# Optimization experiments

Hardware: AMD Instinct MI355X
Metric: run time of the kernel (lower is better)

The kernel has to match this reference:

```python
import jax, jax.numpy as jnp
import numpy as np

HEADS = 8
DIM_HEAD = 64
SCALE = DIM_HEAD ** -0.5
QUERY_DIM = 512
CTX_DIM = 64
INNER = HEADS * DIM_HEAD  # 512
GATE_HID = 32


def setup_inputs() -> dict:
    key = jax.random.key(0)
    ks = jax.random.split(key, 11)
    B, N, M = 4, 2048, 2048
    s = lambda fan: 1.0 / np.sqrt(fan)
    return {
        "x": jax.random.normal(ks[0], (B, N, QUERY_DIM), dtype=jnp.float32),
        "context": jax.random.normal(ks[1], (B, M, CTX_DIM), dtype=jnp.float32),
        "Wq": jax.random.normal(ks[2], (QUERY_DIM, INNER), dtype=jnp.float32) * s(QUERY_DIM),
        "Wk": jax.random.normal(ks[3], (CTX_DIM, INNER), dtype=jnp.float32) * s(CTX_DIM),
        "Wv": jax.random.normal(ks[4], (CTX_DIM, INNER), dtype=jnp.float32) * s(CTX_DIM),
        "W1": jax.random.normal(ks[5], (CTX_DIM, GATE_HID), dtype=jnp.float32) * s(CTX_DIM),
        "b1": jnp.zeros((GATE_HID,), dtype=jnp.float32),
        "W2": jax.random.normal(ks[6], (GATE_HID, 1), dtype=jnp.float32) * s(GATE_HID),
        "b2": jnp.zeros((1,), dtype=jnp.float32),
        "Wo": jax.random.normal(ks[7], (INNER, QUERY_DIM), dtype=jnp.float32) * s(INNER),
        "bo": jnp.zeros((QUERY_DIM,), dtype=jnp.float32),
    }


def reference(x, context, Wq, Wk, Wv, W1, b1, W2, b2, Wo, bo):
    B, N, _ = x.shape
    M = context.shape[1]
    # visual reliability gate: sigmoid(relu(ctx @ W1 + b1) @ W2 + b2) -> [B, M, 1]
    gate = jax.nn.sigmoid(jax.nn.relu(context @ W1 + b1) @ W2 + b2)
    ctx = context * gate
    # projections
    q = (x @ Wq).reshape(B, N, HEADS, DIM_HEAD).transpose(0, 2, 1, 3)    # [B,H,N,D]
    k = (ctx @ Wk).reshape(B, M, HEADS, DIM_HEAD).transpose(0, 2, 1, 3)  # [B,H,M,D]
    v = (ctx @ Wv).reshape(B, M, HEADS, DIM_HEAD).transpose(0, 2, 1, 3)  # [B,H,M,D]
    # scaled dot-product attention (full score matrix, as in source)
    sim = jnp.einsum('bhid,bhjd->bhij', q, k) * SCALE
    attn = jax.nn.softmax(sim, axis=-1)
    out = jnp.einsum('bhij,bhjd->bhid', attn, v)
    out = out.transpose(0, 2, 1, 3).reshape(B, N, INNER)
    return out @ Wo + bo
```

## Files before the change

kernel.cpp:

```cpp
#include <hip/hip_runtime.h>

typedef unsigned short u16;
typedef unsigned int u32;
using frag16 = __attribute__((ext_vector_type(8))) short;
using facc   = __attribute__((ext_vector_type(4))) float;
using facc16 = __attribute__((ext_vector_type(16))) float;

#define DEV static __device__ __forceinline__

DEV u16 f2bf(float f) {
  union { float f; unsigned u; } v; v.f = f;
  unsigned r = v.u + 0x7fffu + ((v.u >> 16) & 1u);
  return (u16)(r >> 16);
}
DEV unsigned fbits(float f) {
  union { float f; unsigned u; } v; v.f = f;
  return v.u;
}
DEV unsigned pkbf(float lo, float hi) {
  return __builtin_amdgcn_perm(fbits(hi) + 0x8000u, fbits(lo) + 0x8000u, 0x07060302u);
}
DEV void gld16(const u16* g, u16* l) {
  __builtin_amdgcn_global_load_lds(
      (__attribute__((address_space(1))) unsigned int*)(g),
      (__attribute__((address_space(3))) unsigned int*)(l), 16, 0, 0);
}

__global__ __launch_bounds__(256) void wtrans_all(
    const float* __restrict__ Wq, const float* __restrict__ Wk,
    const float* __restrict__ Wv, const float* __restrict__ Wo,
    u16* __restrict__ WqT, u16* __restrict__ WkT,
    u16* __restrict__ WvT, u16* __restrict__ WoT) {
  int id = blockIdx.x * 256 + threadIdx.x;
  const float* W; u16* WT; int K, idx;
  if (id < 262144)      { W = Wq; WT = WqT; K = 512; idx = id; }
  else if (id < 294912) { W = Wk; WT = WkT; K = 64;  idx = id - 262144; }
  else if (id < 327680) { W = Wv; WT = WvT; K = 64;  idx = id - 294912; }
  else                  { W = Wo; WT = WoT; K = 512; idx = id - 327680; }
  int n = idx / K, k = idx - n * K;
  WT[idx] = f2bf(W[k * 512 + n]);
}

__global__ void cvt_kernel(const float4* __restrict__ x, u16* __restrict__ xb, int n4) {
  int id = blockIdx.x * 256 + threadIdx.x;
  if (id >= n4) return;
  float4 v = x[id];
  ushort4 o;
  o.x = f2bf(v.x); o.y = f2bf(v.y); o.z = f2bf(v.z); o.w = f2bf(v.w);
  *(ushort4*)(xb + (size_t)id * 4) = o;
}

__global__ __launch_bounds__(256) void gate_kernel(const float* __restrict__ ctx,
    const float* __restrict__ W1, const float* __restrict__ b1,
    const float* __restrict__ W2, const float* __restrict__ b2,
    u16* __restrict__ gctx) {
  int wave = threadIdx.x >> 6, lane = threadIdx.x & 63;
  int row = blockIdx.x * 4 + wave;
  __shared__ float sc[4][64];
  float cv = ctx[(size_t)row * 64 + lane];
  sc[wave][lane] = cv;
  __syncthreads();
  float h = 0.f;
  if (lane < 32) {
    h = b1[lane];
    #pragma unroll
    for (int i = 0; i < 64; ++i) h += sc[wave][i] * W1[i * 32 + lane];
    h = fmaxf(h, 0.f) * W2[lane];
  }
  #pragma unroll
  for (int off = 32; off; off >>= 1) h += __shfl_xor(h, off);
  float g = 1.f / (1.f + __expf(-(h + b2[0])));
  gctx[(size_t)row * 64 + lane] = f2bf(cv * g);
}

template<int MODE>
__global__ __launch_bounds__(256) void gemm128(const u16* __restrict__ A,
    const u16* __restrict__ BT, void* __restrict__ Cp,
    const float* __restrict__ bias, int N, float scale) {
  const int K = 512;
  const int lane = threadIdx.x & 63, wave = threadIdx.x >> 6;
  const int quad = lane >> 4, l16 = lane & 15;
  const int wr = wave >> 1, wc = wave & 1;
  const int m0 = blockIdx.y * 128, n0 = blockIdx.x * 64;

  __shared__ __align__(16) u16 As[128 * 32];
  __shared__ __align__(16) u16 Bs[64 * 32];

  const u16* gA = A + (size_t)(m0 + wave * 32 + (lane >> 2)) * K + (lane & 3) * 8;
  const u16* gB = BT + (size_t)(n0 + wave * 16 + (lane >> 2)) * K + (lane & 3) * 8;
  u16* lA0 = As + wave * 1024;
  u16* lA1 = As + wave * 1024 + 512;
  u16* lB  = Bs + wave * 512;

  facc acc[4][2] = {};

  for (int k0 = 0; k0 < K; k0 += 32) {
    if (k0) __syncthreads();
    gld16(gA + k0, lA0);
    gld16(gA + 16 * K + k0, lA1);
    gld16(gB + k0, lB);
    __syncthreads();

    frag16 af[4], bf[2];
    #pragma unroll
    for (int rt = 0; rt < 4; ++rt)
      af[rt] = *(const frag16*)(As + (wr * 64 + rt * 16 + l16) * 32 + quad * 8);
    #pragma unroll
    for (int ct = 0; ct < 2; ++ct)
      bf[ct] = *(const frag16*)(Bs + (wc * 32 + ct * 16 + l16) * 32 + quad * 8);
    #pragma unroll
    for (int rt = 0; rt < 4; ++rt)
      #pragma unroll
      for (int ct = 0; ct < 2; ++ct)
        acc[rt][ct] = __builtin_amdgcn_mfma_f32_16x16x32_bf16(af[rt], bf[ct], acc[rt][ct], 0, 0, 0);
  }

  #pragma unroll
  for (int rt = 0; rt < 4; ++rt) {
    #pragma unroll
    for (int ct = 0; ct < 2; ++ct) {
      int col = n0 + wc * 32 + ct * 16 + l16;
      int r0g = m0 + wr * 64 + rt * 16 + quad * 4;
      if (MODE == 0) {
        u16* C = (u16*)Cp;
        #pragma unroll
        for (int r = 0; r < 4; ++r)
          C[(size_t)(r0g + r) * N + col] = f2bf(acc[rt][ct][r] * scale);
      } else {
        float* C = (float*)Cp;
        float bv = bias[col];
        #pragma unroll
        for (int r = 0; r < 4; ++r)
          C[(size_t)(r0g + r) * N + col] = acc[rt][ct][r] + bv;
      }
    }
  }
}

template<int MODE>
__global__ __launch_bounds__(256) void gemm_bt(const u16* __restrict__ A,
    const u16* __restrict__ BT, void* __restrict__ Cp, int M, int N, int K) {
  int lane = threadIdx.x & 63, wave = threadIdx.x >> 6;
  int quad = lane >> 4, l16 = lane & 15;
  int wr = wave >> 1, wc = wave & 1;
  int rowBase = blockIdx.y * 64 + wr * 32;
  int colBase = blockIdx.x * 64 + wc * 32;
  facc acc[2][2] = {};
  const u16* a0 = A + (size_t)(rowBase + l16) * K + quad * 8;
  const u16* a1 = a0 + (size_t)16 * K;
  const u16* b0 = BT + (size_t)(colBase + l16) * K + quad * 8;
  const u16* b1p = b0 + (size_t)16 * K;
  for (int kk = 0; kk < K; kk += 32) {
    frag16 af0 = *(const frag16*)(a0 + kk);
    frag16 af1 = *(const frag16*)(a1 + kk);
    frag16 bf0 = *(const frag16*)(b0 + kk);
    frag16 bf1 = *(const frag16*)(b1p + kk);
    acc[0][0] = __builtin_amdgcn_mfma_f32_16x16x32_bf16(af0, bf0, acc[0][0], 0, 0, 0);
    acc[0][1] = __builtin_amdgcn_mfma_f32_16x16x32_bf16(af0, bf1, acc[0][1], 0, 0, 0);
    acc[1][0] = __builtin_amdgcn_mfma_f32_16x16x32_bf16(af1, bf0, acc[1][0], 0, 0, 0);
    acc[1][1] = __builtin_amdgcn_mfma_f32_16x16x32_bf16(af1, bf1, acc[1][1], 0, 0, 0);
  }
  #pragma unroll
  for (int rt = 0; rt < 2; ++rt) {
    #pragma unroll
    for (int ct = 0; ct < 2; ++ct) {
      int col = colBase + ct * 16 + l16;
      int r0g = rowBase + rt * 16 + quad * 4;
      if (MODE == 3) {
        u16* C = (u16*)Cp;
        int hh = col >> 6, d = col & 63;
        int b = r0g >> 11;
        #pragma unroll
        for (int r = 0; r < 4; ++r) {
          int m = (r0g + r) & 2047;
          size_t addr = ((((size_t)(b * 8 + hh) * 64 + (m >> 5)) * 4 + (d >> 4)) * 64
                         + ((d >> 3) & 1) * 32 + (m & 31)) * 8 + (d & 7);
          C[addr] = f2bf(acc[rt][ct][r]);
        }
      } else {
        u16* C = (u16*)Cp;
        int hh = col >> 6, d = col & 63;
        int b = r0g >> 11;
        int m = r0g & 2047;
        size_t addr = ((((size_t)(b * 8 + hh) * 64 + (m >> 5)) * 4
                        + ((m >> 4) & 1) * 2 + (d >> 5)) * 64
                       + ((m >> 3) & 1) * 32 + (d & 31)) * 8 + (m & 7);
        ushort4 o;
        o.x = f2bf(acc[rt][ct][0]); o.y = f2bf(acc[rt][ct][1]);
        o.z = f2bf(acc[rt][ct][2]); o.w = f2bf(acc[rt][ct][3]);
        *(ushort4*)(C + addr) = o;
      }
    }
  }
}

__global__ __launch_bounds__(256, 3) void attn_kernel(
    const u16* __restrict__ qb, const u16* __restrict__ Kp,
    const u16* __restrict__ Vp, float* __restrict__ Opart,
    float* __restrict__ Lpart) {
  const int lane = threadIdx.x & 63, wave = threadIdx.x >> 6;
  const int l32 = lane & 31;
  const int hi = lane >> 5;
  const int bid = blockIdx.x;
  const int bh = bid & 31;
  const int qblk = (bid >> 5) & 15;
  const int js = bid >> 9;
  const int b = bh >> 3, h = bh & 7;
  const int q0 = (qblk * 4 + wave) * 32;
  const int rowg = b * 2048 + q0 + l32;

  const u16* qp = qb + (size_t)rowg * 512 + h * 64 + hi * 8;
  frag16 qf0 = *(const frag16*)(qp);
  frag16 qf1 = *(const frag16*)(qp + 16);
  frag16 qf2 = *(const frag16*)(qp + 32);
  frag16 qf3 = *(const frag16*)(qp + 48);

  facc16 O0 = {}, O1 = {};
  float lsum = 0.f;

  const size_t ts = 2048;
  const u16* kpb = Kp + (size_t)(bh * 64 + js * 32) * ts + lane * 8;
  const u16* vpb = Vp + (size_t)(bh * 64 + js * 32) * ts + lane * 8;

  for (int t = 0; t < 32; ++t) {
    const u16* kt = kpb + (size_t)t * ts;
    frag16 kf0 = *(const frag16*)(kt);
    frag16 kf1 = *(const frag16*)(kt + 512);
    frag16 kf2 = *(const frag16*)(kt + 1024);
    frag16 kf3 = *(const frag16*)(kt + 1536);
    const u16* vt = vpb + (size_t)t * ts;
    frag16 vf00 = *(const frag16*)(vt);
    frag16 vf01 = *(const frag16*)(vt + 512);
    frag16 vf10 = *(const frag16*)(vt + 1024);
    frag16 vf11 = *(const frag16*)(vt + 1536);

    facc16 S = {};
    S = __builtin_amdgcn_mfma_f32_32x32x16_bf16(kf0, qf0, S, 0, 0, 0);
    S = __builtin_amdgcn_mfma_f32_32x32x16_bf16(kf1, qf1, S, 0, 0, 0);
    S = __builtin_amdgcn_mfma_f32_32x32x16_bf16(kf2, qf2, S, 0, 0, 0);
    S = __builtin_amdgcn_mfma_f32_32x32x16_bf16(kf3, qf3, S, 0, 0, 0);

    float e[16];
    #pragma unroll
    for (int r = 0; r < 16; ++r) e[r] = __builtin_amdgcn_exp2f(S[r]);
    #pragma unroll
    for (int r = 0; r < 16; ++r) lsum += e[r];

    unsigned pu[2][4];
    #pragma unroll
    for (int c = 0; c < 2; ++c) {
      const float* ee = e + c * 8;
      unsigned L0 = pkbf(ee[0], ee[1]);
      unsigned L1 = pkbf(ee[2], ee[3]);
      unsigned H0 = pkbf(ee[4], ee[5]);
      unsigned H1 = pkbf(ee[6], ee[7]);
      unsigned Y0 = hi ? L0 : H0;
      unsigned Y1 = hi ? L1 : H1;
      unsigned X0 = (unsigned)__shfl_xor((int)Y0, 32);
      unsigned X1 = (unsigned)__shfl_xor((int)Y1, 32);
      pu[c][0] = hi ? X0 : L0;
      pu[c][1] = hi ? X1 : L1;
      pu[c][2] = hi ? H0 : X0;
      pu[c][3] = hi ? H1 : X1;
    }
    frag16 P0 = *(frag16*)&pu[0][0];
    frag16 P1 = *(frag16*)&pu[1][0];

    O0 = __builtin_amdgcn_mfma_f32_32x32x16_bf16(vf00, P0, O0, 0, 0, 0);
    O0 = __builtin_amdgcn_mfma_f32_32x32x16_bf16(vf10, P1, O0, 0, 0, 0);
    O1 = __builtin_amdgcn_mfma_f32_32x32x16_bf16(vf01, P0, O1, 0, 0, 0);
    O1 = __builtin_amdgcn_mfma_f32_32x32x16_bf16(vf11, P1, O1, 0, 0, 0);
  }

  lsum += __shfl_xor(lsum, 32);

  float* op = Opart + ((size_t)js * 8192 + rowg) * 512 + h * 64;
  #pragma unroll
  for (int dt = 0; dt < 2; ++dt) {
    #pragma unroll
    for (int rq = 0; rq < 4; ++rq) {
      float4 v;
      if (dt == 0) { v.x = O0[rq*4]; v.y = O0[rq*4+1]; v.z = O0[rq*4+2]; v.w = O0[rq*4+3]; }
      else         { v.x = O1[rq*4]; v.y = O1[rq*4+1]; v.z = O1[rq*4+2]; v.w = O1[rq*4+3]; }
      int d0 = dt * 32 + 8 * rq + 4 * hi;
      *(float4*)(op + d0) = v;
    }
  }
  if (!hi) Lpart[(size_t)js * 65536 + (size_t)rowg * 8 + h] = lsum;
}

__global__ __launch_bounds__(256) void combine_kernel(const float* __restrict__ Opart,
    const float* __restrict__ Lpart, u16* __restrict__ ob) {
  int id = blockIdx.x * 256 + threadIdx.x;
  int row = id >> 7, c4 = (id & 127) * 4;
  int hh = c4 >> 6;
  size_t o = (size_t)row * 512 + c4;
  const float4 o0 = *(const float4*)(Opart + o);
  const float4 o1 = *(const float4*)(Opart + (size_t)8192 * 512 + o);
  float rl = 1.f / (Lpart[(size_t)row * 8 + hh] + Lpart[65536 + (size_t)row * 8 + hh]);
  ushort4 u;
  u.x = f2bf((o0.x + o1.x) * rl);
  u.y = f2bf((o0.y + o1.y) * rl);
  u.z = f2bf((o0.z + o1.z) * rl);
  u.w = f2bf((o0.w + o1.w) * rl);
  *(ushort4*)(ob + o) = u;
}

extern "C" void kernel_launch(void* const* d_in, const int* in_sizes, int n_in,
                              void* d_out, int out_size, void* d_ws, size_t ws_size,
                              hipStream_t stream) {
  const float* x   = (const float*)d_in[0];
  const float* ctx = (const float*)d_in[1];
  const float* Wq  = (const float*)d_in[2];
  const float* Wk  = (const float*)d_in[3];
  const float* Wv  = (const float*)d_in[4];
  const float* W1  = (const float*)d_in[5];
  const float* b1  = (const float*)d_in[6];
  const float* W2  = (const float*)d_in[7];
  const float* b2  = (const float*)d_in[8];
  const float* Wo  = (const float*)d_in[9];
  const float* bo  = (const float*)d_in[10];
  float* out = (float*)d_out;

  char* ws = (char*)d_ws;
  size_t off = 0;
  auto alloc = [&](size_t bytes) {
    char* p = ws + off;
    off += (bytes + 255) & ~(size_t)255;
    return p;
  };
  u16* xb    = (u16*)alloc(8192ull * 512 * 2);
  u16* qb    = (u16*)alloc(8192ull * 512 * 2);
  u16* Kp    = (u16*)alloc(8192ull * 512 * 2);
  u16* Vp    = (u16*)alloc(8192ull * 512 * 2);
  u16* ob    = (u16*)alloc(8192ull * 512 * 2);
  u16* gctx  = (u16*)alloc(8192ull * 64 * 2);
  u16* WqT   = (u16*)alloc(512ull * 512 * 2);
  u16* WkT   = (u16*)alloc(512ull * 64 * 2);
  u16* WvT   = (u16*)alloc(512ull * 64 * 2);
  u16* WoT   = (u16*)alloc(512ull * 512 * 2);
  float* Opart = (float*)alloc(2ull * 8192 * 512 * 4);
  float* Lpart = (float*)alloc(2ull * 65536 * 4);

  wtrans_all<<<2304, 256, 0, stream>>>(Wq, Wk, Wv, Wo, WqT, WkT, WvT, WoT);
  cvt_kernel<<<4096, 256, 0, stream>>>((const float4*)x, xb, 8192 * 512 / 4);
  gate_kernel<<<2048, 256, 0, stream>>>(ctx, W1, b1, W2, b2, gctx);

  gemm128<0><<<dim3(8, 64), 256, 0, stream>>>(xb, WqT, qb, nullptr, 512,
                                              0.125f * 1.4426950408889634f);
  gemm_bt<3><<<dim3(8, 128), 256, 0, stream>>>(gctx, WkT, Kp, 8192, 512, 64);
  gemm_bt<4><<<dim3(8, 128), 256, 0, stream>>>(gctx, WvT, Vp, 8192, 512, 64);

  attn_kernel<<<1024, 256, 0, stream>>>(qb, Kp, Vp, Opart, Lpart);
  combine_kernel<<<4096, 256, 0, stream>>>(Opart, Lpart, ob);

  gemm128<2><<<dim3(8, 64), 256, 0, stream>>>(ob, WoT, out, bo, 512, 1.f);
}
```

Measured before the change: 197.8 us.

## Fuse prep and K/V GEMM launches, deepen GEMM k-step, prefetch attention tiles

```diff
diff --git a/kernel.cpp b/kernel.cpp
--- a/kernel.cpp
+++ b/kernel.cpp
@@ -26,28 +26,28 @@
       (__attribute__((address_space(3))) unsigned int*)(l), 16, 0, 0);
 }
 
-__global__ __launch_bounds__(256) void wtrans_all(
+__global__ __launch_bounds__(256) void prep_kernel(const float4* __restrict__ x,
     const float* __restrict__ Wq, const float* __restrict__ Wk,
     const float* __restrict__ Wv, const float* __restrict__ Wo,
-    u16* __restrict__ WqT, u16* __restrict__ WkT,
+    u16* __restrict__ xb, u16* __restrict__ WqT, u16* __restrict__ WkT,
     u16* __restrict__ WvT, u16* __restrict__ WoT) {
-  int id = blockIdx.x * 256 + threadIdx.x;
-  const float* W; u16* WT; int K, idx;
-  if (id < 262144)      { W = Wq; WT = WqT; K = 512; idx = id; }
-  else if (id < 294912) { W = Wk; WT = WkT; K = 64;  idx = id - 262144; }
-  else if (id < 327680) { W = Wv; WT = WvT; K = 64;  idx = id - 294912; }
-  else                  { W = Wo; WT = WoT; K = 512; idx = id - 327680; }
-  int n = idx / K, k = idx - n * K;
-  WT[idx] = f2bf(W[k * 512 + n]);
-}
-
-__global__ void cvt_kernel(const float4* __restrict__ x, u16* __restrict__ xb, int n4) {
-  int id = blockIdx.x * 256 + threadIdx.x;
-  if (id >= n4) return;
-  float4 v = x[id];
-  ushort4 o;
-  o.x = f2bf(v.x); o.y = f2bf(v.y); o.z = f2bf(v.z); o.w = f2bf(v.w);
-  *(ushort4*)(xb + (size_t)id * 4) = o;
+  int bid = blockIdx.x;
+  if (bid < 4096) {
+    int id = bid * 256 + threadIdx.x;
+    float4 v = x[id];
+    ushort4 o;
+    o.x = f2bf(v.x); o.y = f2bf(v.y); o.z = f2bf(v.z); o.w = f2bf(v.w);
+    *(ushort4*)(xb + (size_t)id * 4) = o;
+  } else {
+    int id = (bid - 4096) * 256 + threadIdx.x;
+    const float* W; u16* WT; int K, idx;
+    if (id < 262144)      { W = Wq; WT = WqT; K = 512; idx = id; }
+    else if (id < 294912) { W = Wk; WT = WkT; K = 64;  idx = id - 262144; }
+    else if (id < 327680) { W = Wv; WT = WvT; K = 64;  idx = id - 294912; }
+    else                  { W = Wo; WT = WoT; K = 512; idx = id - 327680; }
+    int n = idx / K, k = idx - n * K;
+    WT[idx] = f2bf(W[k * 512 + n]);
+  }
 }
 
 __global__ __launch_bounds__(256) void gate_kernel(const float* __restrict__ ctx,
@@ -83,36 +83,39 @@
   const int wr = wave >> 1, wc = wave & 1;
   const int m0 = blockIdx.y * 128, n0 = blockIdx.x * 64;
 
-  __shared__ __align__(16) u16 As[128 * 32];
-  __shared__ __align__(16) u16 Bs[64 * 32];
+  __shared__ __align__(16) u16 As[2][128 * 32];
+  __shared__ __align__(16) u16 Bs[2][64 * 32];
 
   const u16* gA = A + (size_t)(m0 + wave * 32 + (lane >> 2)) * K + (lane & 3) * 8;
   const u16* gB = BT + (size_t)(n0 + wave * 16 + (lane >> 2)) * K + (lane & 3) * 8;
-  u16* lA0 = As + wave * 1024;
-  u16* lA1 = As + wave * 1024 + 512;
-  u16* lB  = Bs + wave * 512;
 
   facc acc[4][2] = {};
 
-  for (int k0 = 0; k0 < K; k0 += 32) {
+  for (int k0 = 0; k0 < K; k0 += 64) {
     if (k0) __syncthreads();
-    gld16(gA + k0, lA0);
-    gld16(gA + 16 * K + k0, lA1);
-    gld16(gB + k0, lB);
+    gld16(gA + k0,           As[0] + wave * 1024);
+    gld16(gA + 16 * K + k0,  As[0] + wave * 1024 + 512);
+    gld16(gA + k0 + 32,          As[1] + wave * 1024);
+    gld16(gA + 16 * K + k0 + 32, As[1] + wave * 1024 + 512);
+    gld16(gB + k0,      Bs[0] + wave * 512);
+    gld16(gB + k0 + 32, Bs[1] + wave * 512);
     __syncthreads();
 
-    frag16 af[4], bf[2];
-    #pragma unroll
-    for (int rt = 0; rt < 4; ++rt)
-      af[rt] = *(const frag16*)(As + (wr * 64 + rt * 16 + l16) * 32 + quad * 8);
-    #pragma unroll
-    for (int ct = 0; ct < 2; ++ct)
-      bf[ct] = *(const frag16*)(Bs + (wc * 32 + ct * 16 + l16) * 32 + quad * 8);
-    #pragma unroll
-    for (int rt = 0; rt < 4; ++rt)
+    #pragma unroll
+    for (int hh = 0; hh < 2; ++hh) {
+      frag16 af[4], bf[2];
+      #pragma unroll
+      for (int rt = 0; rt < 4; ++rt)
+        af[rt] = *(const frag16*)(As[hh] + (wr * 64 + rt * 16 + l16) * 32 + quad * 8);
       #pragma unroll
       for (int ct = 0; ct < 2; ++ct)
-        acc[rt][ct] = __builtin_amdgcn_mfma_f32_16x16x32_bf16(af[rt], bf[ct], acc[rt][ct], 0, 0, 0);
+        bf[ct] = *(const frag16*)(Bs[hh] + (wc * 32 + ct * 16 + l16) * 32 + quad * 8);
+      #pragma unroll
+      for (int rt = 0; rt < 4; ++rt)
+        #pragma unroll
+        for (int ct = 0; ct < 2; ++ct)
+          acc[rt][ct] = __builtin_amdgcn_mfma_f32_16x16x32_bf16(af[rt], bf[ct], acc[rt][ct], 0, 0, 0);
+    }
   }
 
   #pragma unroll
@@ -137,28 +140,38 @@
   }
 }
 
-template<int MODE>
-__global__ __launch_bounds__(256) void gemm_bt(const u16* __restrict__ A,
-    const u16* __restrict__ BT, void* __restrict__ Cp, int M, int N, int K) {
+__global__ __launch_bounds__(256) void gemm_kv(const u16* __restrict__ A,
+    const u16* __restrict__ BkT, const u16* __restrict__ BvT,
+    u16* __restrict__ Kp, u16* __restrict__ Vp) {
+  const int Kd = 64, N = 512;
   int lane = threadIdx.x & 63, wave = threadIdx.x >> 6;
   int quad = lane >> 4, l16 = lane & 15;
   int wr = wave >> 1, wc = wave & 1;
   int rowBase = blockIdx.y * 64 + wr * 32;
   int colBase = blockIdx.x * 64 + wc * 32;
-  facc acc[2][2] = {};
-  const u16* a0 = A + (size_t)(rowBase + l16) * K + quad * 8;
-  const u16* a1 = a0 + (size_t)16 * K;
-  const u16* b0 = BT + (size_t)(colBase + l16) * K + quad * 8;
-  const u16* b1p = b0 + (size_t)16 * K;
-  for (int kk = 0; kk < K; kk += 32) {
+  facc ak[2][2] = {}, av[2][2] = {};
+  const u16* a0 = A + (size_t)(rowBase + l16) * Kd + quad * 8;
+  const u16* a1 = a0 + (size_t)16 * Kd;
+  const u16* bk0 = BkT + (size_t)(colBase + l16) * Kd + quad * 8;
+  const u16* bk1 = bk0 + (size_t)16 * Kd;
+  const u16* bv0 = BvT + (size_t)(colBase + l16) * Kd + quad * 8;
+  const u16* bv1 = bv0 + (size_t)16 * Kd;
+  #pragma unroll
+  for (int kk = 0; kk < Kd; kk += 32) {
     frag16 af0 = *(const frag16*)(a0 + kk);
     frag16 af1 = *(const frag16*)(a1 + kk);
-    frag16 bf0 = *(const frag16*)(b0 + kk);
-    frag16 bf1 = *(const frag16*)(b1p + kk);
-    acc[0][0] = __builtin_amdgcn_mfma_f32_16x16x32_bf16(af0, bf0, acc[0][0], 0, 0, 0);
-    acc[0][1] = __builtin_amdgcn_mfma_f32_16x16x32_bf16(af0, bf1, acc[0][1], 0, 0, 0);
-    acc[1][0] = __builtin_amdgcn_mfma_f32_16x16x32_bf16(af1, bf0, acc[1][0], 0, 0, 0);
-    acc[1][1] = __builtin_amdgcn_mfma_f32_16x16x32_bf16(af1, bf1, acc[1][1], 0, 0, 0);
+    frag16 k0 = *(const frag16*)(bk0 + kk);
+    frag16 k1 = *(const frag16*)(bk1 + kk);
+    frag16 v0 = *(const frag16*)(bv0 + kk);
+    frag16 v1 = *(const frag16*)(bv1 + kk);
+    ak[0][0] = __builtin_amdgcn_mfma_f32_16x16x32_bf16(af0, k0, ak[0][0], 0, 0, 0);
+    ak[0][1] = __builtin_amdgcn_mfma_f32_16x16x32_bf16(af0, k1, ak[0][1], 0, 0, 0);
+    ak[1][0] = __builtin_amdgcn_mfma_f32_16x16x32_bf16(af1, k0, ak[1][0], 0, 0, 0);
+    ak[1][1] = __builtin_amdgcn_mfma_f32_16x16x32_bf16(af1, k1, ak[1][1], 0, 0, 0);
+    av[0][0] = __builtin_amdgcn_mfma_f32_16x16x32_bf16(af0, v0, av[0][0], 0, 0, 0);
+    av[0][1] = __builtin_amdgcn_mfma_f32_16x16x32_bf16(af0, v1, av[0][1], 0, 0, 0);
+    av[1][0] = __builtin_amdgcn_mfma_f32_16x16x32_bf16(af1, v0, av[1][0], 0, 0, 0);
+    av[1][1] = __builtin_amdgcn_mfma_f32_16x16x32_bf16(af1, v1, av[1][1], 0, 0, 0);
   }
   #pragma unroll
   for (int rt = 0; rt < 2; ++rt) {
@@ -166,30 +179,23 @@
     for (int ct = 0; ct < 2; ++ct) {
       int col = colBase + ct * 16 + l16;
       int r0g = rowBase + rt * 16 + quad * 4;
-      if (MODE == 3) {
-        u16* C = (u16*)Cp;
-        int hh = col >> 6, d = col & 63;
-        int b = r0g >> 11;
-        #pragma unroll
-        for (int r = 0; r < 4; ++r) {
-          int m = (r0g + r) & 2047;
-          size_t addr = ((((size_t)(b * 8 + hh) * 64 + (m >> 5)) * 4 + (d >> 4)) * 64
-                         + ((d >> 3) & 1) * 32 + (m & 31)) * 8 + (d & 7);
-          C[addr] = f2bf(acc[rt][ct][r]);
-        }
-      } else {
-        u16* C = (u16*)Cp;
-        int hh = col >> 6, d = col & 63;
-        int b = r0g >> 11;
-        int m = r0g & 2047;
-        size_t addr = ((((size_t)(b * 8 + hh) * 64 + (m >> 5)) * 4
-                        + ((m >> 4) & 1) * 2 + (d >> 5)) * 64
-                       + ((m >> 3) & 1) * 32 + (d & 31)) * 8 + (m & 7);
-        ushort4 o;
-        o.x = f2bf(acc[rt][ct][0]); o.y = f2bf(acc[rt][ct][1]);
-        o.z = f2bf(acc[rt][ct][2]); o.w = f2bf(acc[rt][ct][3]);
-        *(ushort4*)(C + addr) = o;
+      int hh = col >> 6, d = col & 63;
+      int b = r0g >> 11;
+      #pragma unroll
+      for (int r = 0; r < 4; ++r) {
+        int m = (r0g + r) & 2047;
+        size_t addr = ((((size_t)(b * 8 + hh) * 64 + (m >> 5)) * 4 + (d >> 4)) * 64
+                       + ((d >> 3) & 1) * 32 + (m & 31)) * 8 + (d & 7);
+        Kp[addr] = f2bf(ak[rt][ct][r]);
       }
+      int m = r0g & 2047;
+      size_t addr = ((((size_t)(b * 8 + hh) * 64 + (m >> 5)) * 4
+                      + ((m >> 4) & 1) * 2 + (d >> 5)) * 64
+                     + ((m >> 3) & 1) * 32 + (d & 31)) * 8 + (m & 7);
+      ushort4 o;
+      o.x = f2bf(av[rt][ct][0]); o.y = f2bf(av[rt][ct][1]);
+      o.z = f2bf(av[rt][ct][2]); o.w = f2bf(av[rt][ct][3]);
+      *(ushort4*)(Vp + addr) = o;
     }
   }
 }
@@ -222,23 +228,29 @@
   const u16* kpb = Kp + (size_t)(bh * 64 + js * 32) * ts + lane * 8;
   const u16* vpb = Vp + (size_t)(bh * 64 + js * 32) * ts + lane * 8;
 
+  frag16 kf[4], vf[4];
+  #pragma unroll
+  for (int i = 0; i < 4; ++i) {
+    kf[i] = *(const frag16*)(kpb + i * 512);
+    vf[i] = *(const frag16*)(vpb + i * 512);
+  }
+
   for (int t = 0; t < 32; ++t) {
-    const u16* kt = kpb + (size_t)t * ts;
-    frag16 kf0 = *(const frag16*)(kt);
-    frag16 kf1 = *(const frag16*)(kt + 512);
-    frag16 kf2 = *(const frag16*)(kt + 1024);
-    frag16 kf3 = *(const frag16*)(kt + 1536);
-    const u16* vt = vpb + (size_t)t * ts;
-    frag16 vf00 = *(const frag16*)(vt);
-    frag16 vf01 = *(const frag16*)(vt + 512);
-    frag16 vf10 = *(const frag16*)(vt + 1024);
-    frag16 vf11 = *(const frag16*)(vt + 1536);
+    int tn = (t < 31) ? t + 1 : 31;
+    const u16* ktn = kpb + (size_t)tn * ts;
+    const u16* vtn = vpb + (size_t)tn * ts;
+    frag16 nkf[4], nvf[4];
+    #pragma unroll
+    for (int i = 0; i < 4; ++i) {
+      nkf[i] = *(const frag16*)(ktn + i * 512);
+      nvf[i] = *(const frag16*)(vtn + i * 512);
+    }
 
     facc16 S = {};
-    S = __builtin_amdgcn_mfma_f32_32x32x16_bf16(kf0, qf0, S, 0, 0, 0);
-    S = __builtin_amdgcn_mfma_f32_32x32x16_bf16(kf1, qf1, S, 0, 0, 0);
-    S = __builtin_amdgcn_mfma_f32_32x32x16_bf16(kf2, qf2, S, 0, 0, 0);
-    S = __builtin_amdgcn_mfma_f32_32x32x16_bf16(kf3, qf3, S, 0, 0, 0);
+    S = __builtin_amdgcn_mfma_f32_32x32x16_bf16(kf[0], qf0, S, 0, 0, 0);
+    S = __builtin_amdgcn_mfma_f32_32x32x16_bf16(kf[1], qf1, S, 0, 0, 0);
+    S = __builtin_amdgcn_mfma_f32_32x32x16_bf16(kf[2], qf2, S, 0, 0, 0);
+    S = __builtin_amdgcn_mfma_f32_32x32x16_bf16(kf[3], qf3, S, 0, 0, 0);
 
     float e[16];
     #pragma unroll
@@ -266,10 +278,13 @@
     frag16 P0 = *(frag16*)&pu[0][0];
     frag16 P1 = *(frag16*)&pu[1][0];
 
-    O0 = __builtin_amdgcn_mfma_f32_32x32x16_bf16(vf00, P0, O0, 0, 0, 0);
-    O0 = __builtin_amdgcn_mfma_f32_32x32x16_bf16(vf10, P1, O0, 0, 0, 0);
-    O1 = __builtin_amdgcn_mfma_f32_32x32x16_bf16(vf01, P0, O1, 0, 0, 0);
-    O1 = __builtin_amdgcn_mfma_f32_32x32x16_bf16(vf11, P1, O1, 0, 0, 0);
+    O0 = __builtin_amdgcn_mfma_f32_32x32x16_bf16(vf[0], P0, O0, 0, 0, 0);
+    O0 = __builtin_amdgcn_mfma_f32_32x32x16_bf16(vf[2], P1, O0, 0, 0, 0);
+    O1 = __builtin_amdgcn_mfma_f32_32x32x16_bf16(vf[1], P0, O1, 0, 0, 0);
+    O1 = __builtin_amdgcn_mfma_f32_32x32x16_bf16(vf[3], P1, O1, 0, 0, 0);
+
+    #pragma unroll
+    for (int i = 0; i < 4; ++i) { kf[i] = nkf[i]; vf[i] = nvf[i]; }
   }
 
   lsum += __shfl_xor(lsum, 32);
@@ -342,14 +357,13 @@
   float* Opart = (float*)alloc(2ull * 8192 * 512 * 4);
   float* Lpart = (float*)alloc(2ull * 65536 * 4);
 
-  wtrans_all<<<2304, 256, 0, stream>>>(Wq, Wk, Wv, Wo, WqT, WkT, WvT, WoT);
-  cvt_kernel<<<4096, 256, 0, stream>>>((const float4*)x, xb, 8192 * 512 / 4);
+  prep_kernel<<<6400, 256, 0, stream>>>((const float4*)x, Wq, Wk, Wv, Wo,
+                                        xb, WqT, WkT, WvT, WoT);
   gate_kernel<<<2048, 256, 0, stream>>>(ctx, W1, b1, W2, b2, gctx);
 
   gemm128<0><<<dim3(8, 64), 256, 0, stream>>>(xb, WqT, qb, nullptr, 512,
                                               0.125f * 1.4426950408889634f);
-  gemm_bt<3><<<dim3(8, 128), 256, 0, stream>>>(gctx, WkT, Kp, 8192, 512, 64);
-  gemm_bt<4><<<dim3(8, 128), 256, 0, stream>>>(gctx, WvT, Vp, 8192, 512, 64);
+  gemm_kv<<<dim3(8, 128), 256, 0, stream>>>(gctx, WkT, WvT, Kp, Vp);
 
   attn_kernel<<<1024, 256, 0, stream>>>(qb, Kp, Vp, Opart, Lpart);
   combine_kernel<<<4096, 256, 0, stream>>>(Opart, Lpart, ob);
```

Result: faster. 186.7 us (-5.6%).
